# Performance work log

Measured on AMD Instinct MI355X. Metric: run time of the kernel, lower is better.

## Reference

```python
import jax, jax.numpy as jnp
import numpy as np

VOCAB = 256
BIG = 128
NN = 1024  # nodes per LSTM layer


def setup_inputs() -> dict:
    key = jax.random.key(0)
    ks = jax.random.split(key, 10)
    T, B = 512, 128
    in_dim = VOCAB + 2 + 1  # one-hot char + 2 speaker flags + bot flag
    emb = 512

    def w(k, shape, fan_in):
        return jax.random.normal(k, shape, dtype=jnp.float32) * np.float32(1.0 / np.sqrt(fan_in))

    return {
        "inputs": jax.random.normal(ks[0], (T, B, in_dim), dtype=jnp.float32),
        "emb_W": w(ks[1], (in_dim, emb), in_dim),
        "lstm_W0": w(ks[2], (emb + BIG + NN, 4 * NN), emb + BIG + NN),
        "lstm_b0": jnp.zeros((4 * NN,), dtype=jnp.float32),
        "lstm_W1": w(ks[3], (NN + NN, 4 * NN), NN + NN),
        "lstm_b1": jnp.zeros((4 * NN,), dtype=jnp.float32),
        "out_W0": w(ks[4], (NN, NN), NN),
        "out_b0": jnp.zeros((NN,), dtype=jnp.float32),
        "out_W1": w(ks[5], (NN, VOCAB), NN),
        "out_b1": jnp.zeros((VOCAB,), dtype=jnp.float32),
    }


def _lstm_cell(x, h, c, W, b, nn):
    # concat + matmul + bias, split [3nn | nn], sigmoid/tanh gating
    z = jnp.concatenate([x, h], axis=1) @ W + b  # [B, 4nn]
    sigm = jax.nn.sigmoid(z[:, : 3 * nn])
    trans = jnp.tanh(z[:, 3 * nn :])
    f, i, o = sigm[:, :nn], sigm[:, nn : 2 * nn], sigm[:, 2 * nn :]
    c_new = f * c + i * trans
    h_new = o * jnp.tanh(c_new)
    return h_new, c_new


def reference(inputs, emb_W, lstm_W0, lstm_b0, lstm_W1, lstm_b1,
              out_W0, out_b0, out_W1, out_b1):
    T, B, _ = inputs.shape
    first_speaker = jnp.array([[1.0, 0.0]], dtype=inputs.dtype)

    def step(carry, inp_t):
        h0, c0, h1, c1 = carry
        # embed (dropout keep_prob = 1.0)
        emb = inp_t @ emb_W  # [B, emb]
        # attach big flag: +/-1 tile depending on speaker flag == [1, 0]
        flag = inp_t[:, VOCAB : VOCAB + 2]
        comp = jnp.prod((flag == first_speaker).astype(inp_t.dtype), axis=1, keepdims=True)
        comp = jax.lax.stop_gradient(comp)
        big = jnp.tile((comp - 0.5) * 2.0, (1, BIG))  # [B, BIG]
        x = jnp.concatenate([emb, big], axis=1)
        # 2-layer LSTM stack
        h0, c0 = _lstm_cell(x, h0, c0, lstm_W0, lstm_b0, NN)
        h1, c1 = _lstm_cell(h0, h1, c1, lstm_W1, lstm_b1, NN)
        # output module: Linear -> ReLU -> Linear
        hs = jax.nn.relu(h1 @ out_W0 + out_b0)
        logits = hs @ out_W1 + out_b1  # [B, VOCAB]
        return (h0, c0, h1, c1), logits

    zeros = jnp.zeros((B, NN), dtype=inputs.dtype)
    init = (zeros, zeros, zeros, zeros)
    _, logits = jax.lax.scan(step, init, inputs)  # [T, B, VOCAB]
    return logits
```

## Files before the change

kernel.cpp:

```cpp
#include <hip/hip_runtime.h>
#include <hip/hip_bf16.h>
#include <math.h>

typedef unsigned short u16;
typedef short short8v __attribute__((ext_vector_type(8)));
typedef float f32x4 __attribute__((ext_vector_type(4)));

#define TT 512
#define BB 128
#define IND 259
#define KPWF 384

#define LDS_BYTES 73728

__device__ __forceinline__ u16 f2bf(float x) {
    __hip_bfloat16 h = __float2bfloat16(x);
    return *reinterpret_cast<u16*>(&h);
}
__device__ __forceinline__ float bf2f(u16 u) {
    unsigned v = ((unsigned)u) << 16;
    return __uint_as_float(v);
}
__device__ __forceinline__ void splitbf(float x, u16& hi, u16& lo) {
    hi = f2bf(x);
    lo = f2bf(x - bf2f(hi));
}

__global__ __launch_bounds__(256) void k_zero(float* __restrict__ p, int n) {
    int i = blockIdx.x * 256 + threadIdx.x;
    int stride = gridDim.x * 256;
    for (; i < n; i += stride) p[i] = 0.f;
}

__global__ __launch_bounds__(256) void k_fold(const float* __restrict__ embW,
                                              const float* __restrict__ W0,
                                              float* __restrict__ WF) {
    int j = blockIdx.x * 256 + threadIdx.x;
    int i = blockIdx.y;
    float acc = 0.f;
    for (int e = 0; e < 512; ++e)
        acc += embW[i * 512 + e] * W0[(size_t)e * 4096 + j];
    WF[(size_t)i * 4096 + j] = acc;
}

__global__ __launch_bounds__(256) void k_S(const float* __restrict__ W0, float* __restrict__ S) {
    int j = blockIdx.x * 256 + threadIdx.x;
    float acc = 0.f;
    for (int r = 0; r < 128; ++r)
        acc += W0[(size_t)(512 + r) * 4096 + j];
    S[j] = acc;
}

__global__ __launch_bounds__(256) void k_sgn(const float* __restrict__ inp, float* __restrict__ sgn) {
    int i = blockIdx.x * 256 + threadIdx.x;
    float f0 = inp[(size_t)i * IND + 256];
    float f1 = inp[(size_t)i * IND + 257];
    sgn[i] = (f0 == 1.0f && f1 == 0.0f) ? 1.0f : -1.0f;
}

__global__ __launch_bounds__(256) void k_split(const float* __restrict__ src, int srcStride,
                                               int K, int Kpad, int perm,
                                               u16* __restrict__ hi, u16* __restrict__ lo) {
    int col = blockIdx.y;
    int k = blockIdx.x * 256 + threadIdx.x;
    if (k >= Kpad) return;
    int j = col;
    if (perm) {
        int c = col & 15, g = (col >> 4) & 3, hs = col >> 6;
        j = g * 1024 + hs * 16 + c;
    }
    float v = (k < K) ? src[(size_t)k * srcStride + j] : 0.f;
    u16 h, l; splitbf(v, h, l);
    hi[(size_t)col * Kpad + k] = h;
    lo[(size_t)col * Kpad + k] = l;
}

template<int NC, int AMODE>
__device__ __forceinline__ void gemm_core(
    char* smem, int tid,
    const u16* Ah0, const u16* Al0,
    const u16* Ah1, const u16* Al1,
    int phsw,
    const float* Af,
    const u16* Bh, const u16* Bl, int ldb,
    int bmode, int bhalf,
    int nkt,
    f32x4 (&acc)[2][NC/32])
{
    constexpr int ROWB = 144;
    constexpr int APL  = 64 * ROWB;
    constexpr int BPL  = NC * ROWB;
    constexpr int BUFB = 2 * APL + 2 * BPL;
    const int lane = tid & 63, wid = tid >> 6;
    const int wrg = wid >> 1, wcg = wid & 1;
    const int rlo = lane & 15, khi = lane >> 4;

    const int srow = tid >> 2;
    const int skE  = (tid & 3) * 16;
    int bcol, bplane, bq;
    if (NC == 64) { bcol = tid >> 2; int bs = tid & 3; bplane = bs >> 1; bq = bs & 1; }
    else          { bcol = tid >> 3; int bs = tid & 7; bplane = bs >> 2; bq = bs & 3; }
    int bcg = bcol;
    if (bmode) bcg = ((bcol >> 3) * 16) + bhalf * 8 + (bcol & 7);

    uint4 rah0, rah1, ral0, ral1, rb0, rb1, rb2, rb3;
    float rf[16];

    auto LOADF = [&](int tile) {
        if constexpr (AMODE == 0) {
            const u16* pAh = Ah0; const u16* pAl = Al0; int kk = tile * 64;
            if (tile >= phsw) { pAh = Ah1; pAl = Al1; kk = (tile - phsw) * 64; }
            const u16* pa = pAh + (size_t)srow * 1024 + kk + skE;
            rah0 = *(const uint4*)(pa);
            rah1 = *(const uint4*)(pa + 8);
            const u16* pl = pAl + (size_t)srow * 1024 + kk + skE;
            ral0 = *(const uint4*)(pl);
            ral1 = *(const uint4*)(pl + 8);
        } else {
            const float* sa = Af + (size_t)srow * IND;
            int k0 = tile * 64 + skE;
            #pragma unroll
            for (int j = 0; j < 16; ++j) rf[j] = (k0 + j < IND) ? sa[k0 + j] : 0.f;
        }
        const u16* bp = bplane ? Bl : Bh;
        if constexpr (NC == 64) {
            const u16* s = bp + (size_t)bcg * ldb + tile * 64 + bq * 32;
            rb0 = *(const uint4*)(s);
            rb1 = *(const uint4*)(s + 8);
            rb2 = *(const uint4*)(s + 16);
            rb3 = *(const uint4*)(s + 24);
        } else {
            const u16* s = bp + (size_t)bcg * ldb + tile * 64 + bq * 16;
            rb0 = *(const uint4*)(s);
            rb1 = *(const uint4*)(s + 8);
        }
    };
    auto WRITEF = [&](int tile) {
        char* buf = smem + (tile & 1) * BUFB;
        char* d = buf + srow * ROWB + skE * 2;
        if constexpr (AMODE == 0) {
            *(uint4*)d = rah0;
            *(uint4*)(d + 16) = rah1;
            *(uint4*)(d + APL) = ral0;
            *(uint4*)(d + APL + 16) = ral1;
        } else {
            alignas(16) u16 hb[16], lb[16];
            #pragma unroll
            for (int j = 0; j < 16; ++j) splitbf(rf[j], hb[j], lb[j]);
            *(uint4*)d = *(const uint4*)hb;
            *(uint4*)(d + 16) = *(const uint4*)(hb + 8);
            *(uint4*)(d + APL) = *(const uint4*)lb;
            *(uint4*)(d + APL + 16) = *(const uint4*)(lb + 8);
        }
        char* e = buf + 2 * APL + bplane * BPL + bcol * ROWB;
        if constexpr (NC == 64) {
            char* p = e + bq * 64;
            *(uint4*)(p)      = rb0;
            *(uint4*)(p + 16) = rb1;
            *(uint4*)(p + 32) = rb2;
            *(uint4*)(p + 48) = rb3;
        } else {
            char* p = e + bq * 32;
            *(uint4*)(p)      = rb0;
            *(uint4*)(p + 16) = rb1;
        }
    };
    auto COMPUTEF = [&](int kt) {
        const char* buf = smem + (kt & 1) * BUFB;
        #pragma unroll
        for (int ks = 0; ks < 2; ++ks) {
            short8v ah[2], al[2], bh[NC/32], bl[NC/32];
            #pragma unroll
            for (int rfi = 0; rfi < 2; ++rfi) {
                int row = wrg * 32 + rfi * 16 + rlo;
                const char* p = buf + row * ROWB + ks * 64 + khi * 16;
                ah[rfi] = *(const short8v*)p;
                al[rfi] = *(const short8v*)(p + APL);
            }
            #pragma unroll
            for (int cfi = 0; cfi < NC/32; ++cfi) {
                int col = wcg * (NC/2) + cfi * 16 + rlo;
                const char* q = buf + 2 * APL + col * ROWB + ks * 64 + khi * 16;
                bh[cfi] = *(const short8v*)q;
                bl[cfi] = *(const short8v*)(q + BPL);
            }
            #pragma unroll
            for (int rfi = 0; rfi < 2; ++rfi)
                #pragma unroll
                for (int cfi = 0; cfi < NC/32; ++cfi) {
                    acc[rfi][cfi] = __builtin_amdgcn_mfma_f32_16x16x32_bf16(ah[rfi], bh[cfi], acc[rfi][cfi], 0, 0, 0);
                    acc[rfi][cfi] = __builtin_amdgcn_mfma_f32_16x16x32_bf16(ah[rfi], bl[cfi], acc[rfi][cfi], 0, 0, 0);
                    acc[rfi][cfi] = __builtin_amdgcn_mfma_f32_16x16x32_bf16(al[rfi], bh[cfi], acc[rfi][cfi], 0, 0, 0);
                }
        }
    };

    LOADF(0); WRITEF(0); __syncthreads();
    for (int kt = 0; kt < nkt; ++kt) {
        if (kt + 1 < nkt) LOADF(kt + 1);
        COMPUTEF(kt);
        if (kt + 1 < nkt) WRITEF(kt + 1);
        __syncthreads();
    }
}

template<int NC>
__device__ __forceinline__ void store_zs(char* smem, int tid, f32x4 (&acc)[2][NC/32], int ncp) {
    float* zs = (float*)smem;
    const int lane = tid & 63, wid = tid >> 6;
    const int wrg = wid >> 1, wcg = wid & 1;
    const int rlo = lane & 15, khi = lane >> 4;
    #pragma unroll
    for (int rfi = 0; rfi < 2; ++rfi)
        #pragma unroll
        for (int cfi = 0; cfi < NC/32; ++cfi)
            #pragma unroll
            for (int r = 0; r < 4; ++r)
                zs[(wrg*32 + rfi*16 + khi*4 + r) * ncp + wcg*(NC/2) + cfi*16 + rlo] = acc[rfi][cfi][r];
}

struct SArgs {
    const float *inp, *Sv, *SG, *b0, *b1;
    const u16 *WFh, *WFl, *W0h, *W0l, *W1h, *W1l;
    u16 *h0h0, *h0l0, *h0h1, *h0l1;
    u16 *ringh, *ringl;
    float *Zin, *c0, *c1;
    int R, t;
};

__global__ __launch_bounds__(256) void k_step(SArgs a) {
    extern __shared__ char smem[];
    const int bid = blockIdx.x, tid = threadIdx.x;
    const int t = a.t;

    if (bid < 128) {
        if (t < 0 || t >= TT) return;
        const int mb = bid >> 6, hs = bid & 63;
        const int m0 = mb * 64;
        f32x4 acc[2][2];
        #pragma unroll
        for (int i = 0; i < 2; ++i) { acc[i][0] = (f32x4)0.f; acc[i][1] = (f32x4)0.f; }
        const u16* Ah = (((t - 1) & 1) ? a.h0h1 : a.h0h0) + (size_t)m0 * 1024;
        const u16* Al = (((t - 1) & 1) ? a.h0l1 : a.h0l0) + (size_t)m0 * 1024;
        gemm_core<64,0>(smem, tid, Ah, Al, Ah, Al, 99, nullptr,
                        a.W0h + (size_t)hs*64*1024, a.W0l + (size_t)hs*64*1024, 1024,
                        0, 0, 16, acc);
        store_zs<64>(smem, tid, acc, 68);
        __syncthreads();
        float* zs = (float*)smem;
        const float* zin = a.Zin + (size_t)(t & 1) * BB * 4096;
        u16* hoh = ((t & 1) ? a.h0h1 : a.h0h0);
        u16* hol = ((t & 1) ? a.h0l1 : a.h0l0);
        #pragma unroll
        for (int i = 0; i < 4; ++i) {
            int q = tid + 256 * i;
            int row = q >> 4, c16 = q & 15;
            int grow = m0 + row;
            int hid = hs * 16 + c16;
            float sg = a.SG[(size_t)t * BB + grow];
            const float* zr = zs + row * 68;
            const float* zn = zin + (size_t)grow * 4096 + hs * 64;
            float zF = zr[c16]      + zn[c16]      + sg * a.Sv[hid]        + a.b0[hid];
            float zI = zr[16 + c16] + zn[16 + c16] + sg * a.Sv[1024 + hid] + a.b0[1024 + hid];
            float zO = zr[32 + c16] + zn[32 + c16] + sg * a.Sv[2048 + hid] + a.b0[2048 + hid];
            float zG = zr[48 + c16] + zn[48 + c16] + sg * a.Sv[3072 + hid] + a.b0[3072 + hid];
            float f = 1.f / (1.f + expf(-zF));
            float ii = 1.f / (1.f + expf(-zI));
            float o = 1.f / (1.f + expf(-zO));
            float g = tanhf(zG);
            size_t ci = (size_t)grow * 1024 + hid;
            float cn = f * a.c0[ci] + ii * g;
            a.c0[ci] = cn;
            float h = o * tanhf(cn);
            u16 hh, hl; splitbf(h, hh, hl);
            hoh[ci] = hh; hol[ci] = hl;
        }
    } else if (bid < 384) {
        const int tau = t - 1;
        if (tau < 0 || tau >= TT) return;
        const int bb = bid - 128;
        const int mb = bb >> 7, sub = bb & 127;
        const int hs = sub >> 1, half = sub & 1;
        const int m0 = mb * 64;
        f32x4 acc[2][1];
        #pragma unroll
        for (int i = 0; i < 2; ++i) acc[i][0] = (f32x4)0.f;
        const u16* A0h = (((tau & 1) ? a.h0h1 : a.h0h0)) + (size_t)m0 * 1024;
        const u16* A0l = (((tau & 1) ? a.h0l1 : a.h0l0)) + (size_t)m0 * 1024;
        int slotr = (tau - 1 + a.R) % a.R;
        const u16* A1h = a.ringh + (size_t)slotr * BB * 1024 + (size_t)m0 * 1024;
        const u16* A1l = a.ringl + (size_t)slotr * BB * 1024 + (size_t)m0 * 1024;
        gemm_core<32,0>(smem, tid, A0h, A0l, A1h, A1l, 16, nullptr,
                        a.W1h + (size_t)hs*64*2048, a.W1l + (size_t)hs*64*2048, 2048,
                        1, half, 32, acc);
        store_zs<32>(smem, tid, acc, 36);
        __syncthreads();
        float* zs = (float*)smem;
        int slotw = tau % a.R;
        u16* rh = a.ringh + (size_t)slotw * BB * 1024;
        u16* rl = a.ringl + (size_t)slotw * BB * 1024;
        #pragma unroll
        for (int i = 0; i < 2; ++i) {
            int q = tid + 256 * i;
            int row = q >> 3, c8 = q & 7;
            int grow = m0 + row;
            int hid = hs * 16 + half * 8 + c8;
            const float* zr = zs + row * 36;
            float zF = zr[c8]      + a.b1[hid];
            float zI = zr[8 + c8]  + a.b1[1024 + hid];
            float zO = zr[16 + c8] + a.b1[2048 + hid];
            float zG = zr[24 + c8] + a.b1[3072 + hid];
            float f = 1.f / (1.f + expf(-zF));
            float ii = 1.f / (1.f + expf(-zI));
            float o = 1.f / (1.f + expf(-zO));
            float g = tanhf(zG);
            size_t ci = (size_t)grow * 1024 + hid;
            float cn = f * a.c1[ci] + ii * g;
            a.c1[ci] = cn;
            float h = o * tanhf(cn);
            u16 hh, hl; splitbf(h, hh, hl);
            rh[ci] = hh; rl[ci] = hl;
        }
    } else {
        const int tz = t + 1;
        if (tz < 0 || tz >= TT) return;
        const int zb = bid - 384;
        const int mb = zb >> 6, cwg = zb & 63;
        const int m0 = mb * 64;
        const int col0 = cwg * 64;
        f32x4 acc[2][2];
        #pragma unroll
        for (int i = 0; i < 2; ++i) { acc[i][0] = (f32x4)0.f; acc[i][1] = (f32x4)0.f; }
        const float* Af = a.inp + (size_t)tz * BB * IND + (size_t)m0 * IND;
        gemm_core<64,1>(smem, tid, nullptr, nullptr, nullptr, nullptr, 999, Af,
                        a.WFh + (size_t)col0 * KPWF, a.WFl + (size_t)col0 * KPWF, KPWF,
                        0, 0, KPWF / 64, acc);
        float* zo = a.Zin + (size_t)(tz & 1) * BB * 4096;
        const int lane = tid & 63, wid = tid >> 6;
        const int wrg = wid >> 1, wcg = wid & 1;
        const int rlo = lane & 15, khi = lane >> 4;
        #pragma unroll
        for (int rfi = 0; rfi < 2; ++rfi)
            #pragma unroll
            for (int cfi = 0; cfi < 2; ++cfi)
                #pragma unroll
                for (int r = 0; r < 4; ++r)
                    zo[(size_t)(m0 + wrg*32 + rfi*16 + khi*4 + r) * 4096 + col0 + wcg*32 + cfi*16 + rlo] = acc[rfi][cfi][r];
    }
}

__global__ __launch_bounds__(256) void k_head1(const u16* __restrict__ ringh, const u16* __restrict__ ringl,
                                               const u16* __restrict__ Wh, const u16* __restrict__ Wl,
                                               const float* __restrict__ bias,
                                               u16* __restrict__ hsh, u16* __restrict__ hsl) {
    extern __shared__ char smem[];
    const int tid = threadIdx.x;
    const int nb = blockIdx.x, mb = blockIdx.y;
    const size_t m0 = (size_t)mb * 64;
    f32x4 acc[2][2];
    #pragma unroll
    for (int i = 0; i < 2; ++i) { acc[i][0] = (f32x4)0.f; acc[i][1] = (f32x4)0.f; }
    const u16* Ah = ringh + m0 * 1024;
    const u16* Al = ringl + m0 * 1024;
    gemm_core<64,0>(smem, tid, Ah, Al, Ah, Al, 99, nullptr,
                    Wh + (size_t)nb*64*1024, Wl + (size_t)nb*64*1024, 1024,
                    0, 0, 16, acc);
    const int lane = tid & 63, wid = tid >> 6;
    const int wrg = wid >> 1, wcg = wid & 1;
    const int rlo = lane & 15, khi = lane >> 4;
    #pragma unroll
    for (int rfi = 0; rfi < 2; ++rfi)
        #pragma unroll
        for (int cfi = 0; cfi < 2; ++cfi)
            #pragma unroll
            for (int r = 0; r < 4; ++r) {
                int row = wrg*32 + rfi*16 + khi*4 + r;
                int col = nb*64 + wcg*32 + cfi*16 + rlo;
                float v = acc[rfi][cfi][r] + bias[col];
                v = fmaxf(v, 0.f);
                u16 hh, hl; splitbf(v, hh, hl);
                size_t o = (m0 + row) * 1024 + col;
                hsh[o] = hh; hsl[o] = hl;
            }
}

__global__ __launch_bounds__(256) void k_head2(const u16* __restrict__ hsh, const u16* __restrict__ hsl,
                                               const u16* __restrict__ Wh, const u16* __restrict__ Wl,
                                               const float* __restrict__ bias,
                                               float* __restrict__ outp) {
    extern __shared__ char smem[];
    const int tid = threadIdx.x;
    const int nb = blockIdx.x, mb = blockIdx.y;
    const size_t m0 = (size_t)mb * 64;
    f32x4 acc[2][2];
    #pragma unroll
    for (int i = 0; i < 2; ++i) { acc[i][0] = (f32x4)0.f; acc[i][1] = (f32x4)0.f; }
    const u16* Ah = hsh + m0 * 1024;
    const u16* Al = hsl + m0 * 1024;
    gemm_core<64,0>(smem, tid, Ah, Al, Ah, Al, 99, nullptr,
                    Wh + (size_t)nb*64*1024, Wl + (size_t)nb*64*1024, 1024,
                    0, 0, 16, acc);
    const int lane = tid & 63, wid = tid >> 6;
    const int wrg = wid >> 1, wcg = wid & 1;
    const int rlo = lane & 15, khi = lane >> 4;
    #pragma unroll
    for (int rfi = 0; rfi < 2; ++rfi)
        #pragma unroll
        for (int cfi = 0; cfi < 2; ++cfi)
            #pragma unroll
            for (int r = 0; r < 4; ++r) {
                int row = wrg*32 + rfi*16 + khi*4 + r;
                int col = nb*64 + wcg*32 + cfi*16 + rlo;
                outp[(m0 + row) * 256 + col] = acc[rfi][cfi][r] + bias[col];
            }
}

extern "C" void kernel_launch(void* const* d_in, const int* in_sizes, int n_in,
                              void* d_out, int out_size, void* d_ws, size_t ws_size,
                              hipStream_t stream)
{
    (void)in_sizes; (void)n_in; (void)out_size;
    const float* inputs = (const float*)d_in[0];
    const float* embW   = (const float*)d_in[1];
    const float* W0     = (const float*)d_in[2];
    const float* b0     = (const float*)d_in[3];
    const float* W1     = (const float*)d_in[4];
    const float* b1     = (const float*)d_in[5];
    const float* oW0    = (const float*)d_in[6];
    const float* ob0    = (const float*)d_in[7];
    const float* oW1    = (const float*)d_in[8];
    const float* ob1    = (const float*)d_in[9];
    float* out = (float*)d_out;

    char* base = (char*)d_ws;
    size_t off = 0;
    auto take = [&](size_t n) -> char* {
        size_t a = (off + 255) & ~(size_t)255;
        char* r = base + a;
        off = a + n;
        return r;
    };

    u16* WFh = (u16*)take(4096ull * KPWF * 2);
    u16* WFl = (u16*)take(4096ull * KPWF * 2);
    u16* W0h = (u16*)take(4096ull * 1024 * 2);
    u16* W0l = (u16*)take(4096ull * 1024 * 2);
    u16* W1h = (u16*)take(4096ull * 2048 * 2);
    u16* W1l = (u16*)take(4096ull * 2048 * 2);
    u16* oWAh = (u16*)take(1024ull * 1024 * 2);
    u16* oWAl = (u16*)take(1024ull * 1024 * 2);
    u16* oWBh = (u16*)take(256ull * 1024 * 2);
    u16* oWBl = (u16*)take(256ull * 1024 * 2);
    float* WFfold = (float*)take(259ull * 4096 * 4);
    float* Sv = (float*)take(4096 * 4);
    float* SG = (float*)take((size_t)TT * BB * 4);
    float* Zin = (float*)take(2ull * BB * 4096 * 4);
    u16* h0h0 = (u16*)take((size_t)BB * 1024 * 2);
    u16* h0l0 = (u16*)take((size_t)BB * 1024 * 2);
    u16* h0h1 = (u16*)take((size_t)BB * 1024 * 2);
    u16* h0l1 = (u16*)take((size_t)BB * 1024 * 2);
    float* c0 = (float*)take((size_t)BB * 1024 * 4);
    float* c1 = (float*)take((size_t)BB * 1024 * 4);

    size_t avail = (ws_size > off + (1u << 20)) ? (ws_size - off - (1u << 20)) : 0;
    int R = 512;
    while (R > 2 && (size_t)R * (BB * 1024ull * 2 * 4) > avail) R >>= 1;
    u16* ringh = (u16*)take((size_t)R * BB * 1024 * 2);
    u16* ringl = (u16*)take((size_t)R * BB * 1024 * 2);
    u16* hsh   = (u16*)take((size_t)R * BB * 1024 * 2);
    u16* hsl   = (u16*)take((size_t)R * BB * 1024 * 2);

    k_fold<<<dim3(16, 259), 256, 0, stream>>>(embW, W0, WFfold);
    k_S<<<16, 256, 0, stream>>>(W0, Sv);
    k_sgn<<<256, 256, 0, stream>>>(inputs, SG);
    k_split<<<dim3(2, 4096), 256, 0, stream>>>(WFfold, 4096, 259, KPWF, 1, WFh, WFl);
    k_split<<<dim3(4, 4096), 256, 0, stream>>>(W0 + 640ull * 4096, 4096, 1024, 1024, 1, W0h, W0l);
    k_split<<<dim3(8, 4096), 256, 0, stream>>>(W1, 4096, 2048, 2048, 1, W1h, W1l);
    k_split<<<dim3(4, 1024), 256, 0, stream>>>(oW0, 1024, 1024, 1024, 0, oWAh, oWAl);
    k_split<<<dim3(4, 256), 256, 0, stream>>>(oW1, 256, 1024, 1024, 0, oWBh, oWBl);
    k_zero<<<64, 256, 0, stream>>>(c0, BB * 1024);
    k_zero<<<64, 256, 0, stream>>>(c1, BB * 1024);
    k_zero<<<32, 256, 0, stream>>>((float*)h0h1, BB * 1024 / 2);
    k_zero<<<32, 256, 0, stream>>>((float*)h0l1, BB * 1024 / 2);
    k_zero<<<32, 256, 0, stream>>>((float*)(ringh + (size_t)(R - 1) * BB * 1024), BB * 1024 / 2);
    k_zero<<<32, 256, 0, stream>>>((float*)(ringl + (size_t)(R - 1) * BB * 1024), BB * 1024 / 2);

    SArgs a;
    a.inp = inputs; a.Sv = Sv; a.SG = SG; a.b0 = b0; a.b1 = b1;
    a.WFh = WFh; a.WFl = WFl; a.W0h = W0h; a.W0l = W0l; a.W1h = W1h; a.W1l = W1l;
    a.h0h0 = h0h0; a.h0l0 = h0l0; a.h0h1 = h0h1; a.h0l1 = h0l1;
    a.ringh = ringh; a.ringl = ringl;
    a.Zin = Zin; a.c0 = c0; a.c1 = c1;
    a.R = R;

    for (int L = -1; L <= TT; ++L) {
        a.t = L;
        k_step<<<512, 256, LDS_BYTES, stream>>>(a);
        if (L >= 1 && (L % R) == 0) {
            int c = L / R - 1;
            k_head1<<<dim3(16, R * 2), 256, LDS_BYTES, stream>>>(ringh, ringl, oWAh, oWAl, ob0, hsh, hsl);
            k_head2<<<dim3(4, R * 2), 256, LDS_BYTES, stream>>>(hsh, hsl, oWBh, oWBl, ob1,
                                                                out + (size_t)c * R * BB * 256);
        }
    }
}
```

Baseline: 18.70 ms.

## Split recurrent step into split-K 128x128 GEMM kernel and separate gate kernel

```diff
diff --git a/kernel.cpp b/kernel.cpp
--- a/kernel.cpp
+++ b/kernel.cpp
@@ -11,7 +11,10 @@
 #define IND 259
 #define KPWF 384
 
-#define LDS_BYTES 73728
+#define APL 18432
+#define GBUFB 73728
+#define LDS_G 147456
+#define LDS_H 73728
 
 __device__ __forceinline__ u16 f2bf(float x) {
     __hip_bfloat16 h = __float2bfloat16(x);
@@ -25,6 +28,7 @@
     hi = f2bf(x);
     lo = f2bf(x - bf2f(hi));
 }
+__device__ __forceinline__ float sigm(float x) { return 1.f / (1.f + expf(-x)); }
 
 __global__ __launch_bounds__(256) void k_zero(float* __restrict__ p, int n) {
     int i = blockIdx.x * 256 + threadIdx.x;
@@ -75,26 +79,291 @@
     lo[(size_t)col * Kpad + k] = l;
 }
 
+template<int AMODE>
+__device__ __forceinline__ void gemm128(
+    char* smem, int tid,
+    const u16* Ah, const u16* Al, int lda,
+    const float* Af, int kmax,
+    const u16* Bh, const u16* Bl, int ldb,
+    int ntiles,
+    f32x4 (&acc)[4][4])
+{
+    const int lane = tid & 63, wid = tid >> 6;
+    const int wrg = wid >> 1, wcg = wid & 1;
+    const int rlo = lane & 15, khi = lane >> 4;
+
+    const int srow = tid >> 1;
+    const int sh   = tid & 1;
+
+    uint4 rah[4], ral[4], rbh[4], rbl[4];
+    float rf[32];
+
+    auto LOADF = [&](int tile) {
+        if constexpr (AMODE == 0) {
+            const u16* pa = Ah + (size_t)srow * lda + tile * 64 + sh * 32;
+            const u16* pl = Al + (size_t)srow * lda + tile * 64 + sh * 32;
+            #pragma unroll
+            for (int j = 0; j < 4; ++j) {
+                rah[j] = *(const uint4*)(pa + j * 8);
+                ral[j] = *(const uint4*)(pl + j * 8);
+            }
+        } else {
+            const float* sa = Af + (size_t)srow * lda;
+            int k0 = tile * 64 + sh * 32;
+            #pragma unroll
+            for (int j = 0; j < 32; ++j) rf[j] = (k0 + j < kmax) ? sa[k0 + j] : 0.f;
+        }
+        const u16* pb = Bh + (size_t)srow * ldb + tile * 64 + sh * 32;
+        const u16* pq = Bl + (size_t)srow * ldb + tile * 64 + sh * 32;
+        #pragma unroll
+        for (int j = 0; j < 4; ++j) {
+            rbh[j] = *(const uint4*)(pb + j * 8);
+            rbl[j] = *(const uint4*)(pq + j * 8);
+        }
+    };
+    auto WRITEF = [&](int tile) {
+        char* buf = smem + (tile & 1) * GBUFB;
+        char* da = buf + srow * 144 + sh * 64;
+        if constexpr (AMODE == 0) {
+            #pragma unroll
+            for (int j = 0; j < 4; ++j) {
+                *(uint4*)(da + j * 16) = rah[j];
+                *(uint4*)(da + APL + j * 16) = ral[j];
+            }
+        } else {
+            alignas(16) u16 hb[32], lb[32];
+            #pragma unroll
+            for (int j = 0; j < 32; ++j) splitbf(rf[j], hb[j], lb[j]);
+            #pragma unroll
+            for (int j = 0; j < 4; ++j) {
+                *(uint4*)(da + j * 16) = *(const uint4*)(hb + j * 8);
+                *(uint4*)(da + APL + j * 16) = *(const uint4*)(lb + j * 8);
+            }
+        }
+        char* db = buf + 2 * APL + srow * 144 + sh * 64;
+        #pragma unroll
+        for (int j = 0; j < 4; ++j) {
+            *(uint4*)(db + j * 16) = rbh[j];
+            *(uint4*)(db + APL + j * 16) = rbl[j];
+        }
+    };
+    auto COMPUTEF = [&](int kt) {
+        const char* buf = smem + (kt & 1) * GBUFB;
+        #pragma unroll
+        for (int ks = 0; ks < 2; ++ks) {
+            short8v ah[4], al[4];
+            #pragma unroll
+            for (int rfi = 0; rfi < 4; ++rfi) {
+                int row = wrg * 64 + rfi * 16 + rlo;
+                const char* p = buf + row * 144 + ks * 64 + khi * 16;
+                ah[rfi] = *(const short8v*)p;
+                al[rfi] = *(const short8v*)(p + APL);
+            }
+            #pragma unroll
+            for (int cfi = 0; cfi < 4; ++cfi) {
+                int col = wcg * 64 + cfi * 16 + rlo;
+                const char* q = buf + 2 * APL + col * 144 + ks * 64 + khi * 16;
+                short8v bh = *(const short8v*)q;
+                short8v bl = *(const short8v*)(q + APL);
+                #pragma unroll
+                for (int rfi = 0; rfi < 4; ++rfi) {
+                    acc[rfi][cfi] = __builtin_amdgcn_mfma_f32_16x16x32_bf16(ah[rfi], bh, acc[rfi][cfi], 0, 0, 0);
+                    acc[rfi][cfi] = __builtin_amdgcn_mfma_f32_16x16x32_bf16(ah[rfi], bl, acc[rfi][cfi], 0, 0, 0);
+                    acc[rfi][cfi] = __builtin_amdgcn_mfma_f32_16x16x32_bf16(al[rfi], bh, acc[rfi][cfi], 0, 0, 0);
+                }
+            }
+        }
+    };
+
+    LOADF(0); WRITEF(0); __syncthreads();
+    for (int kt = 0; kt < ntiles; ++kt) {
+        if (kt + 1 < ntiles) LOADF(kt + 1);
+        COMPUTEF(kt);
+        if (kt + 1 < ntiles) WRITEF(kt + 1);
+        __syncthreads();
+    }
+}
+
+__device__ __forceinline__ void store_acc128(float* __restrict__ out, int col0, int tid,
+                                             f32x4 (&acc)[4][4]) {
+    const int lane = tid & 63, wid = tid >> 6;
+    const int wrg = wid >> 1, wcg = wid & 1;
+    const int rlo = lane & 15, khi = lane >> 4;
+    #pragma unroll
+    for (int rfi = 0; rfi < 4; ++rfi)
+        #pragma unroll
+        for (int cfi = 0; cfi < 4; ++cfi)
+            #pragma unroll
+            for (int r = 0; r < 4; ++r)
+                out[(size_t)(wrg*64 + rfi*16 + khi*4 + r) * 4096 + col0 + wcg*64 + cfi*16 + rlo] = acc[rfi][cfi][r];
+}
+
+struct GArgs {
+    const float* inp;
+    const u16 *WFh, *WFl, *W0h, *W0l, *W1h, *W1l;
+    const u16 *h0h0, *h0l0, *h0h1, *h0l1;
+    const u16 *ringh, *ringl;
+    float *P0, *P1, *Zin;
+    int R, t;
+};
+
+__global__ __launch_bounds__(256) void k_gemm(GArgs a) {
+    extern __shared__ char smem[];
+    const int bid = blockIdx.x, tid = threadIdx.x;
+    const int t = a.t;
+    f32x4 acc[4][4];
+    #pragma unroll
+    for (int i = 0; i < 4; ++i)
+        #pragma unroll
+        for (int j = 0; j < 4; ++j) acc[i][j] = (f32x4)0.f;
+
+    if (bid < 64) {
+        if (t < 0 || t >= TT) return;
+        const int cb = bid >> 1, s = bid & 1;
+        const u16* Ah = (((t - 1) & 1) ? a.h0h1 : a.h0h0) + s * 512;
+        const u16* Al = (((t - 1) & 1) ? a.h0l1 : a.h0l0) + s * 512;
+        gemm128<0>(smem, tid, Ah, Al, 1024, nullptr, 0,
+                   a.W0h + (size_t)(cb * 128) * 1024 + s * 512,
+                   a.W0l + (size_t)(cb * 128) * 1024 + s * 512, 1024, 8, acc);
+        store_acc128(a.P0 + (size_t)s * BB * 4096, cb * 128, tid, acc);
+    } else if (bid < 192) {
+        const int tau = t - 1;
+        if (tau < 0 || tau >= TT) return;
+        const int q = bid - 64, cb = q >> 2, s = q & 3;
+        const u16 *Ah, *Al;
+        if (s < 2) {
+            Ah = (((tau & 1) ? a.h0h1 : a.h0h0)) + s * 512;
+            Al = (((tau & 1) ? a.h0l1 : a.h0l0)) + s * 512;
+        } else {
+            int slot = (tau - 1 + a.R) % a.R;
+            Ah = a.ringh + (size_t)slot * BB * 1024 + (s - 2) * 512;
+            Al = a.ringl + (size_t)slot * BB * 1024 + (s - 2) * 512;
+        }
+        gemm128<0>(smem, tid, Ah, Al, 1024, nullptr, 0,
+                   a.W1h + (size_t)(cb * 128) * 2048 + s * 512,
+                   a.W1l + (size_t)(cb * 128) * 2048 + s * 512, 2048, 8, acc);
+        store_acc128(a.P1 + (size_t)s * BB * 4096, cb * 128, tid, acc);
+    } else {
+        const int tz = t + 1;
+        if (tz < 0 || tz >= TT) return;
+        const int cb = bid - 192;
+        gemm128<1>(smem, tid, nullptr, nullptr, IND,
+                   a.inp + (size_t)tz * BB * IND, IND,
+                   a.WFh + (size_t)(cb * 128) * KPWF,
+                   a.WFl + (size_t)(cb * 128) * KPWF, KPWF, 6, acc);
+        store_acc128(a.Zin + (size_t)(tz & 1) * BB * 4096, cb * 128, tid, acc);
+    }
+}
+
+struct TArgs {
+    const float *P0, *P1, *Zin, *Sv, *SG, *b0, *b1;
+    float *c0, *c1;
+    u16 *h0h0, *h0l0, *h0h1, *h0l1, *ringh, *ringl;
+    int R, t;
+};
+
+template<int NS, bool CELL0>
+__device__ __forceinline__ void gate_work(
+    const float* __restrict__ Pb,
+    const float* __restrict__ zin,
+    float sg, const float* __restrict__ Sv,
+    const float* __restrict__ bias,
+    float* __restrict__ cst, u16* __restrict__ oh, u16* __restrict__ ol,
+    int row, int hs)
+{
+    float z[4][16];
+    #pragma unroll
+    for (int g = 0; g < 4; ++g) {
+        #pragma unroll
+        for (int c4 = 0; c4 < 4; ++c4) {
+            float4 v = make_float4(0.f, 0.f, 0.f, 0.f);
+            #pragma unroll
+            for (int s = 0; s < NS; ++s) {
+                float4 p = *(const float4*)(Pb + (size_t)s * BB * 4096 + g * 16 + c4 * 4);
+                v.x += p.x; v.y += p.y; v.z += p.z; v.w += p.w;
+            }
+            if (CELL0) {
+                float4 p = *(const float4*)(zin + g * 16 + c4 * 4);
+                v.x += p.x; v.y += p.y; v.z += p.z; v.w += p.w;
+                float4 sv = *(const float4*)(Sv + g * 1024 + hs * 16 + c4 * 4);
+                v.x += sg * sv.x; v.y += sg * sv.y; v.z += sg * sv.z; v.w += sg * sv.w;
+            }
+            float4 bv = *(const float4*)(bias + g * 1024 + hs * 16 + c4 * 4);
+            v.x += bv.x; v.y += bv.y; v.z += bv.z; v.w += bv.w;
+            z[g][c4*4+0] = v.x; z[g][c4*4+1] = v.y; z[g][c4*4+2] = v.z; z[g][c4*4+3] = v.w;
+        }
+    }
+    alignas(16) u16 hh[16], hl[16];
+    float* cp = cst + (size_t)row * 1024 + hs * 16;
+    #pragma unroll
+    for (int c4 = 0; c4 < 4; ++c4) {
+        float4 cv = *(const float4*)(cp + c4 * 4);
+        float cc[4] = {cv.x, cv.y, cv.z, cv.w};
+        #pragma unroll
+        for (int e = 0; e < 4; ++e) {
+            int c = c4 * 4 + e;
+            float F = sigm(z[0][c]);
+            float I = sigm(z[1][c]);
+            float O = sigm(z[2][c]);
+            float G = tanhf(z[3][c]);
+            float cn = F * cc[e] + I * G;
+            cc[e] = cn;
+            float h = O * tanhf(cn);
+            splitbf(h, hh[c], hl[c]);
+        }
+        *(float4*)(cp + c4 * 4) = make_float4(cc[0], cc[1], cc[2], cc[3]);
+    }
+    u16* ph = oh + (size_t)row * 1024 + hs * 16;
+    u16* pl = ol + (size_t)row * 1024 + hs * 16;
+    *(uint4*)(ph) = *(const uint4*)(hh);
+    *(uint4*)(ph + 8) = *(const uint4*)(hh + 8);
+    *(uint4*)(pl) = *(const uint4*)(hl);
+    *(uint4*)(pl + 8) = *(const uint4*)(hl + 8);
+}
+
+__global__ __launch_bounds__(256) void k_gate(TArgs a) {
+    const int bid = blockIdx.x, tid = threadIdx.x;
+    if (bid < 32) {
+        const int t = a.t;
+        if (t < 0 || t >= TT) return;
+        int q = bid * 256 + tid;
+        int row = q >> 6, hs = q & 63;
+        const float* Pb = a.P0 + (size_t)row * 4096 + hs * 64;
+        const float* zin = a.Zin + (size_t)(t & 1) * BB * 4096 + (size_t)row * 4096 + hs * 64;
+        float sg = a.SG[(size_t)t * BB + row];
+        u16* oh = (t & 1) ? a.h0h1 : a.h0h0;
+        u16* ol = (t & 1) ? a.h0l1 : a.h0l0;
+        gate_work<2, true>(Pb, zin, sg, a.Sv, a.b0, a.c0, oh, ol, row, hs);
+    } else {
+        const int tau = a.t - 1;
+        if (tau < 0 || tau >= TT) return;
+        int q = (bid - 32) * 256 + tid;
+        int row = q >> 6, hs = q & 63;
+        const float* Pb = a.P1 + (size_t)row * 4096 + hs * 64;
+        int slot = tau % a.R;
+        u16* oh = a.ringh + (size_t)slot * BB * 1024;
+        u16* ol = a.ringl + (size_t)slot * BB * 1024;
+        gate_work<4, false>(Pb, nullptr, 0.f, nullptr, a.b1, a.c1, oh, ol, row, hs);
+    }
+}
+
 template<int NC, int AMODE>
 __device__ __forceinline__ void gemm_core(
     char* smem, int tid,
     const u16* Ah0, const u16* Al0,
     const u16* Ah1, const u16* Al1,
-    int phsw,
-    const float* Af,
+    int phsw, const float* Af,
     const u16* Bh, const u16* Bl, int ldb,
-    int bmode, int bhalf,
-    int nkt,
+    int bmode, int bhalf, int nkt,
     f32x4 (&acc)[2][NC/32])
 {
     constexpr int ROWB = 144;
-    constexpr int APL  = 64 * ROWB;
+    constexpr int APL2 = 64 * ROWB;
     constexpr int BPL  = NC * ROWB;
-    constexpr int BUFB = 2 * APL + 2 * BPL;
+    constexpr int BUFB = 2 * APL2 + 2 * BPL;
     const int lane = tid & 63, wid = tid >> 6;
     const int wrg = wid >> 1, wcg = wid & 1;
     const int rlo = lane & 15, khi = lane >> 4;
-
     const int srow = tid >> 2;
     const int skE  = (tid & 3) * 16;
     int bcol, bplane, bq;
@@ -104,24 +373,16 @@
     if (bmode) bcg = ((bcol >> 3) * 16) + bhalf * 8 + (bcol & 7);
 
     uint4 rah0, rah1, ral0, ral1, rb0, rb1, rb2, rb3;
-    float rf[16];
 
     auto LOADF = [&](int tile) {
-        if constexpr (AMODE == 0) {
-            const u16* pAh = Ah0; const u16* pAl = Al0; int kk = tile * 64;
-            if (tile >= phsw) { pAh = Ah1; pAl = Al1; kk = (tile - phsw) * 64; }
-            const u16* pa = pAh + (size_t)srow * 1024 + kk + skE;
-            rah0 = *(const uint4*)(pa);
-            rah1 = *(const uint4*)(pa + 8);
-            const u16* pl = pAl + (size_t)srow * 1024 + kk + skE;
-            ral0 = *(const uint4*)(pl);
-            ral1 = *(const uint4*)(pl + 8);
-        } else {
-            const float* sa = Af + (size_t)srow * IND;
-            int k0 = tile * 64 + skE;
-            #pragma unroll
-            for (int j = 0; j < 16; ++j) rf[j] = (k0 + j < IND) ? sa[k0 + j] : 0.f;
-        }
+        const u16* pAh = Ah0; const u16* pAl = Al0; int kk = tile * 64;
+        if (tile >= phsw) { pAh = Ah1; pAl = Al1; kk = (tile - phsw) * 64; }
+        const u16* pa = pAh + (size_t)srow * 1024 + kk + skE;
+        rah0 = *(const uint4*)(pa);
+        rah1 = *(const uint4*)(pa + 8);
+        const u16* pl = pAl + (size_t)srow * 1024 + kk + skE;
+        ral0 = *(const uint4*)(pl);
+        ral1 = *(const uint4*)(pl + 8);
         const u16* bp = bplane ? Bl : Bh;
         if constexpr (NC == 64) {
             const u16* s = bp + (size_t)bcg * ldb + tile * 64 + bq * 32;
@@ -138,31 +399,18 @@
     auto WRITEF = [&](int tile) {
         char* buf = smem + (tile & 1) * BUFB;
         char* d = buf + srow * ROWB + skE * 2;
-        if constexpr (AMODE == 0) {
-            *(uint4*)d = rah0;
-            *(uint4*)(d + 16) = rah1;
-            *(uint4*)(d + APL) = ral0;
-            *(uint4*)(d + APL + 16) = ral1;
-        } else {
-            alignas(16) u16 hb[16], lb[16];
-            #pragma unroll
-            for (int j = 0; j < 16; ++j) splitbf(rf[j], hb[j], lb[j]);
-            *(uint4*)d = *(const uint4*)hb;
-            *(uint4*)(d + 16) = *(const uint4*)(hb + 8);
-            *(uint4*)(d + APL) = *(const uint4*)lb;
-            *(uint4*)(d + APL + 16) = *(const uint4*)(lb + 8);
-        }
-        char* e = buf + 2 * APL + bplane * BPL + bcol * ROWB;
+        *(uint4*)d = rah0;
+        *(uint4*)(d + 16) = rah1;
+        *(uint4*)(d + APL2) = ral0;
+        *(uint4*)(d + APL2 + 16) = ral1;
+        char* e = buf + 2 * APL2 + bplane * BPL + bcol * ROWB;
         if constexpr (NC == 64) {
             char* p = e + bq * 64;
-            *(uint4*)(p)      = rb0;
-            *(uint4*)(p + 16) = rb1;
-            *(uint4*)(p + 32) = rb2;
-            *(uint4*)(p + 48) = rb3;
+            *(uint4*)(p) = rb0; *(uint4*)(p + 16) = rb1;
+            *(uint4*)(p + 32) = rb2; *(uint4*)(p + 48) = rb3;
         } else {
             char* p = e + bq * 32;
-            *(uint4*)(p)      = rb0;
-            *(uint4*)(p + 16) = rb1;
+            *(uint4*)(p) = rb0; *(uint4*)(p + 16) = rb1;
         }
     };
     auto COMPUTEF = [&](int kt) {
@@ -175,12 +423,12 @@
                 int row = wrg * 32 + rfi * 16 + rlo;
                 const char* p = buf + row * ROWB + ks * 64 + khi * 16;
                 ah[rfi] = *(const short8v*)p;
-                al[rfi] = *(const short8v*)(p + APL);
+                al[rfi] = *(const short8v*)(p + APL2);
             }
             #pragma unroll
             for (int cfi = 0; cfi < NC/32; ++cfi) {
                 int col = wcg * (NC/2) + cfi * 16 + rlo;
-                const char* q = buf + 2 * APL + col * ROWB + ks * 64 + khi * 16;
+                const char* q = buf + 2 * APL2 + col * ROWB + ks * 64 + khi * 16;
                 bh[cfi] = *(const short8v*)q;
                 bl[cfi] = *(const short8v*)(q + BPL);
             }
@@ -201,151 +449,6 @@
         COMPUTEF(kt);
         if (kt + 1 < nkt) WRITEF(kt + 1);
         __syncthreads();
-    }
-}
-
-template<int NC>
-__device__ __forceinline__ void store_zs(char* smem, int tid, f32x4 (&acc)[2][NC/32], int ncp) {
-    float* zs = (float*)smem;
-    const int lane = tid & 63, wid = tid >> 6;
-    const int wrg = wid >> 1, wcg = wid & 1;
-    const int rlo = lane & 15, khi = lane >> 4;
-    #pragma unroll
-    for (int rfi = 0; rfi < 2; ++rfi)
-        #pragma unroll
-        for (int cfi = 0; cfi < NC/32; ++cfi)
-            #pragma unroll
-            for (int r = 0; r < 4; ++r)
-                zs[(wrg*32 + rfi*16 + khi*4 + r) * ncp + wcg*(NC/2) + cfi*16 + rlo] = acc[rfi][cfi][r];
-}
-
-struct SArgs {
-    const float *inp, *Sv, *SG, *b0, *b1;
-    const u16 *WFh, *WFl, *W0h, *W0l, *W1h, *W1l;
-    u16 *h0h0, *h0l0, *h0h1, *h0l1;
-    u16 *ringh, *ringl;
-    float *Zin, *c0, *c1;
-    int R, t;
-};
-
-__global__ __launch_bounds__(256) void k_step(SArgs a) {
-    extern __shared__ char smem[];
-    const int bid = blockIdx.x, tid = threadIdx.x;
-    const int t = a.t;
-
-    if (bid < 128) {
-        if (t < 0 || t >= TT) return;
-        const int mb = bid >> 6, hs = bid & 63;
-        const int m0 = mb * 64;
-        f32x4 acc[2][2];
-        #pragma unroll
-        for (int i = 0; i < 2; ++i) { acc[i][0] = (f32x4)0.f; acc[i][1] = (f32x4)0.f; }
-        const u16* Ah = (((t - 1) & 1) ? a.h0h1 : a.h0h0) + (size_t)m0 * 1024;
-        const u16* Al = (((t - 1) & 1) ? a.h0l1 : a.h0l0) + (size_t)m0 * 1024;
-        gemm_core<64,0>(smem, tid, Ah, Al, Ah, Al, 99, nullptr,
-                        a.W0h + (size_t)hs*64*1024, a.W0l + (size_t)hs*64*1024, 1024,
-                        0, 0, 16, acc);
-        store_zs<64>(smem, tid, acc, 68);
-        __syncthreads();
-        float* zs = (float*)smem;
-        const float* zin = a.Zin + (size_t)(t & 1) * BB * 4096;
-        u16* hoh = ((t & 1) ? a.h0h1 : a.h0h0);
-        u16* hol = ((t & 1) ? a.h0l1 : a.h0l0);
-        #pragma unroll
-        for (int i = 0; i < 4; ++i) {
-            int q = tid + 256 * i;
-            int row = q >> 4, c16 = q & 15;
-            int grow = m0 + row;
-            int hid = hs * 16 + c16;
-            float sg = a.SG[(size_t)t * BB + grow];
-            const float* zr = zs + row * 68;
-            const float* zn = zin + (size_t)grow * 4096 + hs * 64;
-            float zF = zr[c16]      + zn[c16]      + sg * a.Sv[hid]        + a.b0[hid];
-            float zI = zr[16 + c16] + zn[16 + c16] + sg * a.Sv[1024 + hid] + a.b0[1024 + hid];
-            float zO = zr[32 + c16] + zn[32 + c16] + sg * a.Sv[2048 + hid] + a.b0[2048 + hid];
-            float zG = zr[48 + c16] + zn[48 + c16] + sg * a.Sv[3072 + hid] + a.b0[3072 + hid];
-            float f = 1.f / (1.f + expf(-zF));
-            float ii = 1.f / (1.f + expf(-zI));
-            float o = 1.f / (1.f + expf(-zO));
-            float g = tanhf(zG);
-            size_t ci = (size_t)grow * 1024 + hid;
-            float cn = f * a.c0[ci] + ii * g;
-            a.c0[ci] = cn;
-            float h = o * tanhf(cn);
-            u16 hh, hl; splitbf(h, hh, hl);
-            hoh[ci] = hh; hol[ci] = hl;
-        }
-    } else if (bid < 384) {
-        const int tau = t - 1;
-        if (tau < 0 || tau >= TT) return;
-        const int bb = bid - 128;
-        const int mb = bb >> 7, sub = bb & 127;
-        const int hs = sub >> 1, half = sub & 1;
-        const int m0 = mb * 64;
-        f32x4 acc[2][1];
-        #pragma unroll
-        for (int i = 0; i < 2; ++i) acc[i][0] = (f32x4)0.f;
-        const u16* A0h = (((tau & 1) ? a.h0h1 : a.h0h0)) + (size_t)m0 * 1024;
-        const u16* A0l = (((tau & 1) ? a.h0l1 : a.h0l0)) + (size_t)m0 * 1024;
-        int slotr = (tau - 1 + a.R) % a.R;
-        const u16* A1h = a.ringh + (size_t)slotr * BB * 1024 + (size_t)m0 * 1024;
-        const u16* A1l = a.ringl + (size_t)slotr * BB * 1024 + (size_t)m0 * 1024;
-        gemm_core<32,0>(smem, tid, A0h, A0l, A1h, A1l, 16, nullptr,
-                        a.W1h + (size_t)hs*64*2048, a.W1l + (size_t)hs*64*2048, 2048,
-                        1, half, 32, acc);
-        store_zs<32>(smem, tid, acc, 36);
-        __syncthreads();
-        float* zs = (float*)smem;
-        int slotw = tau % a.R;
-        u16* rh = a.ringh + (size_t)slotw * BB * 1024;
-        u16* rl = a.ringl + (size_t)slotw * BB * 1024;
-        #pragma unroll
-        for (int i = 0; i < 2; ++i) {
-            int q = tid + 256 * i;
-            int row = q >> 3, c8 = q & 7;
-            int grow = m0 + row;
-            int hid = hs * 16 + half * 8 + c8;
-            const float* zr = zs + row * 36;
-            float zF = zr[c8]      + a.b1[hid];
-            float zI = zr[8 + c8]  + a.b1[1024 + hid];
-            float zO = zr[16 + c8] + a.b1[2048 + hid];
-            float zG = zr[24 + c8] + a.b1[3072 + hid];
-            float f = 1.f / (1.f + expf(-zF));
-            float ii = 1.f / (1.f + expf(-zI));
-            float o = 1.f / (1.f + expf(-zO));
-            float g = tanhf(zG);
-            size_t ci = (size_t)grow * 1024 + hid;
-            float cn = f * a.c1[ci] + ii * g;
-            a.c1[ci] = cn;
-            float h = o * tanhf(cn);
-            u16 hh, hl; splitbf(h, hh, hl);
-            rh[ci] = hh; rl[ci] = hl;
-        }
-    } else {
-        const int tz = t + 1;
-        if (tz < 0 || tz >= TT) return;
-        const int zb = bid - 384;
-        const int mb = zb >> 6, cwg = zb & 63;
-        const int m0 = mb * 64;
-        const int col0 = cwg * 64;
-        f32x4 acc[2][2];
-        #pragma unroll
-        for (int i = 0; i < 2; ++i) { acc[i][0] = (f32x4)0.f; acc[i][1] = (f32x4)0.f; }
-        const float* Af = a.inp + (size_t)tz * BB * IND + (size_t)m0 * IND;
-        gemm_core<64,1>(smem, tid, nullptr, nullptr, nullptr, nullptr, 999, Af,
-                        a.WFh + (size_t)col0 * KPWF, a.WFl + (size_t)col0 * KPWF, KPWF,
-                        0, 0, KPWF / 64, acc);
-        float* zo = a.Zin + (size_t)(tz & 1) * BB * 4096;
-        const int lane = tid & 63, wid = tid >> 6;
-        const int wrg = wid >> 1, wcg = wid & 1;
-        const int rlo = lane & 15, khi = lane >> 4;
-        #pragma unroll
-        for (int rfi = 0; rfi < 2; ++rfi)
-            #pragma unroll
-            for (int cfi = 0; cfi < 2; ++cfi)
-                #pragma unroll
-                for (int r = 0; r < 4; ++r)
-                    zo[(size_t)(m0 + wrg*32 + rfi*16 + khi*4 + r) * 4096 + col0 + wcg*32 + cfi*16 + rlo] = acc[rfi][cfi][r];
     }
 }
 
@@ -455,6 +558,8 @@
     float* Sv = (float*)take(4096 * 4);
     float* SG = (float*)take((size_t)TT * BB * 4);
     float* Zin = (float*)take(2ull * BB * 4096 * 4);
+    float* P0  = (float*)take(2ull * BB * 4096 * 4);
+    float* P1  = (float*)take(4ull * BB * 4096 * 4);
     u16* h0h0 = (u16*)take((size_t)BB * 1024 * 2);
     u16* h0l0 = (u16*)take((size_t)BB * 1024 * 2);
     u16* h0h1 = (u16*)take((size_t)BB * 1024 * 2);
@@ -485,22 +590,31 @@
     k_zero<<<32, 256, 0, stream>>>((float*)(ringh + (size_t)(R - 1) * BB * 1024), BB * 1024 / 2);
     k_zero<<<32, 256, 0, stream>>>((float*)(ringl + (size_t)(R - 1) * BB * 1024), BB * 1024 / 2);
 
-    SArgs a;
-    a.inp = inputs; a.Sv = Sv; a.SG = SG; a.b0 = b0; a.b1 = b1;
-    a.WFh = WFh; a.WFl = WFl; a.W0h = W0h; a.W0l = W0l; a.W1h = W1h; a.W1l = W1l;
-    a.h0h0 = h0h0; a.h0l0 = h0l0; a.h0h1 = h0h1; a.h0l1 = h0l1;
-    a.ringh = ringh; a.ringl = ringl;
-    a.Zin = Zin; a.c0 = c0; a.c1 = c1;
-    a.R = R;
+    GArgs ga;
+    ga.inp = inputs;
+    ga.WFh = WFh; ga.WFl = WFl; ga.W0h = W0h; ga.W0l = W0l; ga.W1h = W1h; ga.W1l = W1l;
+    ga.h0h0 = h0h0; ga.h0l0 = h0l0; ga.h0h1 = h0h1; ga.h0l1 = h0l1;
+    ga.ringh = ringh; ga.ringl = ringl;
+    ga.P0 = P0; ga.P1 = P1; ga.Zin = Zin;
+    ga.R = R;
+
+    TArgs ta;
+    ta.P0 = P0; ta.P1 = P1; ta.Zin = Zin; ta.Sv = Sv; ta.SG = SG; ta.b0 = b0; ta.b1 = b1;
+    ta.c0 = c0; ta.c1 = c1;
+    ta.h0h0 = h0h0; ta.h0l0 = h0l0; ta.h0h1 = h0h1; ta.h0l1 = h0l1;
+    ta.ringh = ringh; ta.ringl = ringl;
+    ta.R = R;
 
     for (int L = -1; L <= TT; ++L) {
-        a.t = L;
-        k_step<<<512, 256, LDS_BYTES, stream>>>(a);
-        if (L >= 1 && (L % R) == 0) {
+        ga.t = L;
+        k_gemm<<<224, 256, LDS_G, stream>>>(ga);
+        ta.t = L;
+        k_gate<<<64, 256, 0, stream>>>(ta);
+        if (L >= R && (L % R) == 0) {
             int c = L / R - 1;
-            k_head1<<<dim3(16, R * 2), 256, LDS_BYTES, stream>>>(ringh, ringl, oWAh, oWAl, ob0, hsh, hsl);
-            k_head2<<<dim3(4, R * 2), 256, LDS_BYTES, stream>>>(hsh, hsl, oWBh, oWBl, ob1,
-                                                                out + (size_t)c * R * BB * 256);
-        }
-    }
-}
+            k_head1<<<dim3(16, R * 2), 256, LDS_H, stream>>>(ringh, ringl, oWAh, oWAl, ob0, hsh, hsl);
+            k_head2<<<dim3(4, R * 2), 256, LDS_H, stream>>>(hsh, hsl, oWBh, oWBl, ob1,
+                                                            out + (size_t)c * R * BB * 256);
+        }
+    }
+}
```

New measurement: 32.75 ms. +75.1%, slower.
